# Optimization experiments

Measured on AMD Instinct MI355X. Metric: run time of the kernel, lower is better.

The kernel has to match this reference:

```python
import jax, jax.numpy as jnp
import numpy as np

B, S, H = 4, 2048, 1024

def setup_inputs() -> dict:
    key = jax.random.key(0)
    ks = jax.random.split(key, 6)
    scale = 1.0 / np.sqrt(H)
    return {
        "query": jax.random.normal(ks[0], (B, S, H), dtype=jnp.float32),
        "key":   jax.random.normal(ks[1], (B, S, H), dtype=jnp.float32),
        "value": jax.random.normal(ks[2], (B, S, H), dtype=jnp.float32),
        "Wq": jax.random.normal(ks[3], (H, H), dtype=jnp.float32) * scale,
        "Wk": jax.random.normal(ks[4], (H, H), dtype=jnp.float32) * scale,
        "Wv": jax.random.normal(ks[5], (H, H), dtype=jnp.float32) * scale,
    }

def reference(query, key, value, Wq, Wk, Wv):
    # nn.Linear(bias=False): y = x @ W.T
    q = jnp.einsum('bsh,oh->bso', query, Wq)
    k = jnp.einsum('bsh,oh->bso', key, Wk)
    v = jnp.einsum('bsh,oh->bso', value, Wv)
    # full QK^T scores [B, Q, K], scaled by sqrt(hidden_size)
    scores = jnp.einsum('bqh,bkh->bqk', q, k) / jnp.sqrt(jnp.asarray(H, q.dtype))
    attn = jax.nn.softmax(scores, axis=2)
    return jnp.einsum('bqk,bkh->bqh', attn, v)
```

## Files before the change

kernel.cpp:

```cpp
#include <hip/hip_runtime.h>
#include <hip/hip_bf16.h>
#include <stdint.h>

#define BATCH 4
#define SLEN  2048
#define HID   1024

typedef __attribute__((ext_vector_type(8))) short bfrag8;
typedef __attribute__((ext_vector_type(4))) float facc4;
typedef __attribute__((ext_vector_type(4))) unsigned short us4;

__device__ __forceinline__ unsigned short f2b(float f) {
  union { float f; unsigned int i; } x; x.f = f;
  unsigned int r = x.i + 0x7FFFu + ((x.i >> 16) & 1u);
  return (unsigned short)(r >> 16);
}

__device__ __forceinline__ void gl_lds16(const void* g, void* l) {
  __builtin_amdgcn_global_load_lds(
      (const __attribute__((address_space(1))) void*)g,
      (__attribute__((address_space(3))) void*)l, 16, 0, 0);
}

__global__ __launch_bounds__(256) void cast_all(
    const float* __restrict__ q, const float* __restrict__ k,
    const float* __restrict__ v, const float* __restrict__ wq,
    const float* __restrict__ wk, const float* __restrict__ wv,
    us4* __restrict__ dst, float* __restrict__ lsum) {
  if (blockIdx.x < 8) {
    float4 z = {0.f, 0.f, 0.f, 0.f};
    ((float4*)lsum)[blockIdx.x * 256 + threadIdx.x] = z;
  }
  const long i = (long)blockIdx.x * 256 + threadIdx.x;
  const long S1 = 2097152, S2 = 4194304, S3 = 6291456,
             S4 = 6553600, S5 = 6815744;
  const float4* src; long off;
  if (i < S2) {
    if (i < S1) { src = (const float4*)q;  off = i; }
    else        { src = (const float4*)k;  off = i - S1; }
  } else if (i < S3) { src = (const float4*)v;  off = i - S2; }
  else if   (i < S4) { src = (const float4*)wq; off = i - S3; }
  else if   (i < S5) { src = (const float4*)wk; off = i - S4; }
  else               { src = (const float4*)wv; off = i - S5; }
  float4 x = src[off];
  us4 o;
  o.x = f2b(x.x); o.y = f2b(x.y); o.z = f2b(x.z); o.w = f2b(x.w);
  dst[i] = o;
}

__global__ __launch_bounds__(256) void proj3(
    const unsigned short* __restrict__ Xq, const unsigned short* __restrict__ Wqb,
    const unsigned short* __restrict__ Xk, const unsigned short* __restrict__ Wkb,
    const unsigned short* __restrict__ Xv, const unsigned short* __restrict__ Wvb,
    unsigned short* __restrict__ Qb, unsigned short* __restrict__ Kb,
    unsigned short* __restrict__ Vt) {
  const int pid = blockIdx.x;
  const int p2     = (pid & 7) * 192 + (pid >> 3);
  const int g      = p2 >> 9;
  const int within = p2 & 511;

  const unsigned short* A; const unsigned short* B; unsigned short* C;
  long bm, bn; int ldc_;
  if (g == 0)      { A = Xq; B = Wqb; C = Qb; }
  else if (g == 1) { A = Xk; B = Wkb; C = Kb; }
  else             { A = Wvb; B = Xv; C = Vt; }
  if (g < 2) {
    const int gid = within >> 5, rem = within & 31;
    bm = (long)(gid * 4 + (rem & 3)) * 128;
    bn = (long)(rem >> 2) * 128;
    ldc_ = 1024;
  } else {
    const int gid = within >> 8, rem = within & 255;
    bm = (long)(gid * 4 + (rem & 3)) * 128;
    bn = (long)(rem >> 2) * 128;
    ldc_ = 8192;
  }

  __shared__ __align__(16) unsigned short As[128 * 64];
  __shared__ __align__(16) unsigned short Bs[128 * 64];

  const int tid  = threadIdx.x;
  const int lane = tid & 63;
  const int wave = tid >> 6;
  const int wr   = (wave >> 1) * 64;
  const int wc   = (wave & 1) * 64;
  const int ln   = lane & 15;
  const int lq   = lane >> 4;
  const int swz  = ln & 7;

  facc4 acc[4][4] = {};

  const unsigned short* ap[4]; const unsigned short* bp[4];
  unsigned short* asd[4]; unsigned short* bsd[4];
#pragma unroll
  for (int j = 0; j < 4; ++j) {
    const int c   = j * 256 + tid;
    const int row = c >> 3;
    const int src = ((c & 7) ^ (row & 7)) * 8;
    ap[j]  = A + (bm + row) * 1024 + src;
    bp[j]  = B + (bn + row) * 1024 + src;
    asd[j] = &As[c * 8];
    bsd[j] = &Bs[c * 8];
  }

  for (int k0 = 0; k0 < 1024; k0 += 64) {
#pragma unroll
    for (int j = 0; j < 4; ++j) { gl_lds16(ap[j], asd[j]); ap[j] += 64; }
#pragma unroll
    for (int j = 0; j < 4; ++j) { gl_lds16(bp[j], bsd[j]); bp[j] += 64; }
    __syncthreads();

#pragma unroll
    for (int kk = 0; kk < 2; ++kk) {
      bfrag8 af[4], bfr[4];
#pragma unroll
      for (int i = 0; i < 4; ++i)
        af[i] = *(const bfrag8*)&As[(wr + i * 16 + ln) * 64 + ((kk * 4 + lq) ^ swz) * 8];
#pragma unroll
      for (int j = 0; j < 4; ++j)
        bfr[j] = *(const bfrag8*)&Bs[(wc + j * 16 + ln) * 64 + ((kk * 4 + lq) ^ swz) * 8];
#pragma unroll
      for (int i = 0; i < 4; ++i)
#pragma unroll
        for (int j = 0; j < 4; ++j)
          acc[i][j] = __builtin_amdgcn_mfma_f32_16x16x32_bf16(af[i], bfr[j], acc[i][j], 0, 0, 0);
    }
    __syncthreads();
  }

#pragma unroll
  for (int i = 0; i < 4; ++i)
#pragma unroll
    for (int j = 0; j < 4; ++j) {
      const long m = bm + wr + i * 16 + lq * 4;
      const long n = bn + wc + j * 16 + ln;
#pragma unroll
      for (int r = 0; r < 4; ++r)
        C[(m + r) * (long)ldc_ + n] = f2b(acc[i][j][r]);
    }
}

template <int NT>
__device__ __forceinline__ void core256(
    const unsigned short* __restrict__ A, const unsigned short* __restrict__ B,
    const int lda, const int ldb,
    unsigned short* __restrict__ As, unsigned short* __restrict__ Bs,
    facc4 (&acc)[8][4]) {
  const int tid  = threadIdx.x;
  const int lane = tid & 63;
  const int wave = tid >> 6;
  const int wm = wave >> 2;
  const int wn = wave & 3;
  const int ln = lane & 15;
  const int lq = lane >> 4;
  const int swz = ln & 7;

  const int row0 = tid >> 3;
  const int blk  = (tid & 7) ^ (row0 & 7);
  const unsigned short* pA = A + (long)row0 * lda + blk * 8;
  const unsigned short* pB = B + (long)row0 * ldb + blk * 8;
  const long a64 = 64l * lda, b64 = 64l * ldb;
  unsigned short* dA = As + tid * 8;
  unsigned short* dB = Bs + tid * 8;

#define STG_A(h, b, t) do { const unsigned short* g_ = pA + (h) * (a64 * 2) + (long)(t) * 64; \
    gl_lds16(g_,       dA + (b) * 16384 + (h) * 8192); \
    gl_lds16(g_ + a64, dA + (b) * 16384 + (h) * 8192 + 4096); } while (0)
#define STG_B(h, b, t) do { const unsigned short* g_ = pB + (h) * (b64 * 2) + (long)(t) * 64; \
    gl_lds16(g_,       dB + (b) * 16384 + (h) * 8192); \
    gl_lds16(g_ + b64, dB + (b) * 16384 + (h) * 8192 + 4096); } while (0)

  const int o0 = (lq ^ swz) * 8;
  const int o1 = ((4 + lq) ^ swz) * 8;
  const int aOfs = wm * 8192 + ln * 64;
  const int bOfs = (wn >> 1) * 8192 + ((wn & 1) * 64 + ln) * 64;

#define RD_A4(dst, bufb, mb) do { \
  _Pragma("unroll") for (int m_ = 0; m_ < 4; ++m_) { \
    dst[m_][0] = *(const bfrag8*)(As + (bufb) + aOfs + ((mb) + m_) * 1024 + o0); \
    dst[m_][1] = *(const bfrag8*)(As + (bufb) + aOfs + ((mb) + m_) * 1024 + o1); \
  } } while (0)
#define RD_B2(dst, bufb, nb) do { \
  _Pragma("unroll") for (int n_ = 0; n_ < 2; ++n_) { \
    dst[n_][0] = *(const bfrag8*)(Bs + (bufb) + bOfs + ((nb) + n_) * 1024 + o0); \
    dst[n_][1] = *(const bfrag8*)(Bs + (bufb) + bOfs + ((nb) + n_) * 1024 + o1); \
  } } while (0)

#define MFMAQ(AF, BF, MO, NO) do { \
  _Pragma("unroll") for (int m_ = 0; m_ < 4; ++m_) \
  _Pragma("unroll") for (int n_ = 0; n_ < 2; ++n_) { \
    acc[(MO)+m_][(NO)+n_] = __builtin_amdgcn_mfma_f32_16x16x32_bf16( \
        AF[m_][0], BF[n_][0], acc[(MO)+m_][(NO)+n_], 0, 0, 0); \
    acc[(MO)+m_][(NO)+n_] = __builtin_amdgcn_mfma_f32_16x16x32_bf16( \
        AF[m_][1], BF[n_][1], acc[(MO)+m_][(NO)+n_], 0, 0, 0); \
  } } while (0)

#define PH_MID \
  __builtin_amdgcn_s_barrier(); \
  asm volatile("s_waitcnt lgkmcnt(0)" ::: "memory"); \
  __builtin_amdgcn_sched_barrier(0); \
  __builtin_amdgcn_s_setprio(1)
#define PH_END \
  __builtin_amdgcn_s_setprio(0); \
  __builtin_amdgcn_sched_barrier(0); \
  __builtin_amdgcn_s_barrier()

  STG_A(0, 0, 0); STG_A(1, 0, 0); STG_B(0, 0, 0); STG_B(1, 0, 0);
  STG_B(0, 1, 1); STG_B(1, 1, 1);
  asm volatile("s_waitcnt vmcnt(4)" ::: "memory");
  __builtin_amdgcn_s_barrier();

  constexpr int NI = NT / 2;
#pragma unroll 1
  for (int i = 0; i < NI - 1; ++i) {
    const int O1 = 2 * i + 1, E2 = 2 * i + 2, O2 = 2 * i + 3;
    {
      bfrag8 a0[4][2], a1[4][2], b0[2][2], b1[2][2];
      RD_A4(a0, 0, 0); RD_B2(b0, 0, 0); STG_A(0, 1, O1);
      PH_MID; MFMAQ(a0, b0, 0, 0); PH_END;
      RD_B2(b1, 0, 2); STG_A(1, 1, O1);
      PH_MID; MFMAQ(a0, b1, 0, 2); PH_END;
      RD_A4(a1, 0, 4); STG_B(0, 0, E2);
      PH_MID; MFMAQ(a1, b1, 4, 2); PH_END;
      STG_B(1, 0, E2);
      PH_MID; MFMAQ(a1, b0, 4, 0);
      __builtin_amdgcn_s_setprio(0);
      __builtin_amdgcn_sched_barrier(0);
      asm volatile("s_waitcnt vmcnt(4)" ::: "memory");
      __builtin_amdgcn_s_barrier();
    }
    {
      bfrag8 a0[4][2], a1[4][2], b0[2][2], b1[2][2];
      RD_A4(a0, 16384, 0); RD_B2(b0, 16384, 0); STG_A(0, 0, E2);
      PH_MID; MFMAQ(a0, b0, 0, 0); PH_END;
      RD_B2(b1, 16384, 2); STG_A(1, 0, E2);
      PH_MID; MFMAQ(a0, b1, 0, 2); PH_END;
      RD_A4(a1, 16384, 4); STG_B(0, 1, O2);
      PH_MID; MFMAQ(a1, b1, 4, 2); PH_END;
      STG_B(1, 1, O2);
      PH_MID; MFMAQ(a1, b0, 4, 0);
      __builtin_amdgcn_s_setprio(0);
      __builtin_amdgcn_sched_barrier(0);
      asm volatile("s_waitcnt vmcnt(4)" ::: "memory");
      __builtin_amdgcn_s_barrier();
    }
  }
  {
    const int O1 = NT - 1;
    {
      bfrag8 a0[4][2], a1[4][2], b0[2][2], b1[2][2];
      RD_A4(a0, 0, 0); RD_B2(b0, 0, 0); STG_A(0, 1, O1);
      PH_MID; MFMAQ(a0, b0, 0, 0); PH_END;
      RD_B2(b1, 0, 2); STG_A(1, 1, O1);
      PH_MID; MFMAQ(a0, b1, 0, 2); PH_END;
      RD_A4(a1, 0, 4);
      PH_MID; MFMAQ(a1, b1, 4, 2); PH_END;
      PH_MID; MFMAQ(a1, b0, 4, 0);
      __builtin_amdgcn_s_setprio(0);
      __builtin_amdgcn_sched_barrier(0);
      asm volatile("s_waitcnt vmcnt(0)" ::: "memory");
      __builtin_amdgcn_s_barrier();
    }
    {
      bfrag8 a0[4][2], a1[4][2], b0[2][2], b1[2][2];
      RD_A4(a0, 16384, 0); RD_B2(b0, 16384, 0);
      PH_MID; MFMAQ(a0, b0, 0, 0); PH_END;
      RD_B2(b1, 16384, 2);
      PH_MID; MFMAQ(a0, b1, 0, 2); PH_END;
      RD_A4(a1, 16384, 4);
      PH_MID; MFMAQ(a1, b1, 4, 2); PH_END;
      PH_MID; MFMAQ(a1, b0, 4, 0);
      __builtin_amdgcn_s_setprio(0);
    }
  }
#undef PH_MID
#undef PH_END
#undef MFMAQ
#undef RD_A4
#undef RD_B2
#undef STG_A
#undef STG_B
}

__global__ __launch_bounds__(512, 2) void scores256(
    const unsigned short* __restrict__ Q, const unsigned short* __restrict__ Kb,
    unsigned short* __restrict__ P, float* __restrict__ lsum) {
  extern __shared__ unsigned short smem[];
  unsigned short* As = smem;
  unsigned short* Bs = smem + 32768;

  const long z = blockIdx.z;
  const int pid = blockIdx.y * 8 + blockIdx.x;
  const int p2  = (pid & 7) * 8 + (pid >> 3);
  const long bm = (long)(p2 >> 3) * 256;
  const long bn = (long)(p2 & 7) * 256;

  const long SH = (long)SLEN * HID, SS = (long)SLEN * SLEN;
  facc4 acc[8][4] = {};
  core256<HID / 64>(Q + z * SH + bm * 1024, Kb + z * SH + bn * 1024, 1024, 1024,
                    As, Bs, acc);

  unsigned short* Pz = P + z * SS;
  float* lz = lsum + z * SLEN;
  const int lane = threadIdx.x & 63, wave = threadIdx.x >> 6;
  const int wm = wave >> 2, wn = wave & 3;
  const int ln = lane & 15, lq = lane >> 4;
#pragma unroll
  for (int m = 0; m < 8; ++m) {
#pragma unroll
    for (int r = 0; r < 4; ++r) {
      const long q = bm + wm * 128 + m * 16 + lq * 4 + r;
      float rowsum = 0.f;
#pragma unroll
      for (int n = 0; n < 4; ++n) {
        const long kcol = bn + wn * 64 + n * 16 + ln;
        float e = __expf(acc[m][n][r] * 0.03125f);
        Pz[q * (long)SLEN + kcol] = f2b(e);
        rowsum += e;
      }
      rowsum += __shfl_xor(rowsum, 1, 64);
      rowsum += __shfl_xor(rowsum, 2, 64);
      rowsum += __shfl_xor(rowsum, 4, 64);
      rowsum += __shfl_xor(rowsum, 8, 64);
      if (ln == 0) atomicAdd(&lz[q], rowsum);
    }
  }
}

template <int MODE, typename OutT>
__global__ __launch_bounds__(256) void gemm_nt(
    const unsigned short* __restrict__ A, const unsigned short* __restrict__ B,
    OutT* __restrict__ C, int K, int lda, int ldb, int ldc,
    long aStrideZ, long bStrideZ, long cStrideZ, float alpha,
    float* __restrict__ lsum) {
  A += (long)blockIdx.z * aStrideZ;
  B += (long)blockIdx.z * bStrideZ;
  C += (long)blockIdx.z * cStrideZ;
  const long lz = (long)blockIdx.z * SLEN;

  const int nbm = gridDim.x, nbn = gridDim.y;
  const int nb  = nbm * nbn;
  const int pid = blockIdx.y * nbm + blockIdx.x;
  const int p2  = (pid & 7) * (nb >> 3) + (pid >> 3);
  const int GROUP = 4;
  const int gsize = GROUP * nbn;
  const int gid   = p2 / gsize;
  const int rem   = p2 - gid * gsize;
  const long bm = (long)(gid * GROUP + (rem & (GROUP - 1))) * 128;
  const long bn = (long)(rem >> 2) * 128;

  __shared__ __align__(16) unsigned short As[128 * 64];
  __shared__ __align__(16) unsigned short Bs[128 * 64];

  const int tid  = threadIdx.x;
  const int lane = tid & 63;
  const int wave = tid >> 6;
  const int wr   = (wave >> 1) * 64;
  const int wc   = (wave & 1) * 64;
  const int ln   = lane & 15;
  const int lq   = lane >> 4;
  const int swz  = ln & 7;

  facc4 acc[4][4] = {};

  const unsigned short* ap[4]; const unsigned short* bp[4];
  unsigned short* asd[4]; unsigned short* bsd[4];
#pragma unroll
  for (int j = 0; j < 4; ++j) {
    const int c   = j * 256 + tid;
    const int row = c >> 3;
    const int src = ((c & 7) ^ (row & 7)) * 8;
    ap[j]  = A + (bm + row) * (long)lda + src;
    bp[j]  = B + (bn + row) * (long)ldb + src;
    asd[j] = &As[c * 8];
    bsd[j] = &Bs[c * 8];
  }

  for (int k0 = 0; k0 < K; k0 += 64) {
#pragma unroll
    for (int j = 0; j < 4; ++j) { gl_lds16(ap[j], asd[j]); ap[j] += 64; }
#pragma unroll
    for (int j = 0; j < 4; ++j) { gl_lds16(bp[j], bsd[j]); bp[j] += 64; }
    __syncthreads();

#pragma unroll
    for (int kk = 0; kk < 2; ++kk) {
      bfrag8 af[4], bfr[4];
#pragma unroll
      for (int i = 0; i < 4; ++i)
        af[i] = *(const bfrag8*)&As[(wr + i * 16 + ln) * 64 + ((kk * 4 + lq) ^ swz) * 8];
#pragma unroll
      for (int j = 0; j < 4; ++j)
        bfr[j] = *(const bfrag8*)&Bs[(wc + j * 16 + ln) * 64 + ((kk * 4 + lq) ^ swz) * 8];
#pragma unroll
      for (int i = 0; i < 4; ++i)
#pragma unroll
        for (int j = 0; j < 4; ++j)
          acc[i][j] = __builtin_amdgcn_mfma_f32_16x16x32_bf16(af[i], bfr[j], acc[i][j], 0, 0, 0);
    }
    __syncthreads();
  }

  if constexpr (MODE == 1) {
#pragma unroll
    for (int i = 0; i < 4; ++i) {
#pragma unroll
      for (int r = 0; r < 4; ++r) {
        const long m = bm + wr + i * 16 + lq * 4 + r;
        float rowsum = 0.f;
#pragma unroll
        for (int j = 0; j < 4; ++j) {
          const long n = bn + wc + j * 16 + ln;
          float e = __expf(acc[i][j][r] * alpha);
          C[m * (long)ldc + n] = (OutT)f2b(e);
          rowsum += e;
        }
        rowsum += __shfl_xor(rowsum, 1, 64);
        rowsum += __shfl_xor(rowsum, 2, 64);
        rowsum += __shfl_xor(rowsum, 4, 64);
        rowsum += __shfl_xor(rowsum, 8, 64);
        if (ln == 0) atomicAdd(&lsum[lz + m], rowsum);
      }
    }
  } else {
    float inv[16];
#pragma unroll
    for (int i = 0; i < 4; ++i)
#pragma unroll
      for (int r = 0; r < 4; ++r)
        inv[i * 4 + r] = 1.0f / lsum[lz + bm + wr + i * 16 + lq * 4 + r];
#pragma unroll
    for (int i = 0; i < 4; ++i)
#pragma unroll
      for (int j = 0; j < 4; ++j) {
        const long m = bm + wr + i * 16 + lq * 4;
        const long n = bn + wc + j * 16 + ln;
#pragma unroll
        for (int r = 0; r < 4; ++r)
          ((float*)C)[(m + r) * (long)ldc + n] = acc[i][j][r] * inv[i * 4 + r];
      }
  }
}

extern "C" void kernel_launch(void* const* d_in, const int* in_sizes, int n_in,
                              void* d_out, int out_size, void* d_ws, size_t ws_size,
                              hipStream_t stream) {
  const float* q_in = (const float*)d_in[0];
  const float* k_in = (const float*)d_in[1];
  const float* v_in = (const float*)d_in[2];
  const float* wq   = (const float*)d_in[3];
  const float* wk   = (const float*)d_in[4];
  const float* wv   = (const float*)d_in[5];
  float* out = (float*)d_out;

  const long NXH = (long)BATCH * SLEN * HID;
  const long NW  = (long)HID * HID;
  const long SH  = (long)SLEN * HID;
  const long SS  = (long)SLEN * SLEN;

  unsigned short* ws = (unsigned short*)d_ws;
  unsigned short* Xq  = ws;
  unsigned short* Xk  = Xq  + NXH;
  unsigned short* Xv  = Xk  + NXH;
  unsigned short* Wqb = Xv  + NXH;
  unsigned short* Wkb = Wqb + NW;
  unsigned short* Wvb = Wkb + NW;
  unsigned short* Qb  = Wvb + NW;
  unsigned short* Kb  = Qb  + NXH;
  unsigned short* Vt  = Kb  + NXH;
  float*          lsum = (float*)(Vt + NXH);
  unsigned short* P   = Xq;

  static bool attr_done = false;
  if (!attr_done) {
    hipFuncSetAttribute(reinterpret_cast<const void*>(scores256),
                        hipFuncAttributeMaxDynamicSharedMemorySize, 131072);
    attr_done = true;
  }

  cast_all<<<dim3(27648), dim3(256), 0, stream>>>(q_in, k_in, v_in, wq, wk, wv,
                                                  (us4*)ws, lsum);

  proj3<<<dim3(1536), dim3(256), 0, stream>>>(Xq, Wqb, Xk, Wkb, Xv, Wvb,
                                              Qb, Kb, Vt);

  scores256<<<dim3(8, 8, BATCH), dim3(512), 131072, stream>>>(Qb, Kb, P, lsum);

  gemm_nt<2, float><<<dim3(16, 8, BATCH), dim3(256), 0, stream>>>(
      P, Vt, out, SLEN, SLEN, BATCH * SLEN, HID, SS, SLEN, SH, 1.0f, lsum);
}
```

Measured before the change: 277.7 us.

## Fuse all four stages into one persistent cooperative kernel with grid syncs

Replaces the four separate launches (cast, projection, scores, PV) with one cooperative persistent kernel of 256 blocks × 512 threads that runs each stage in turn, separated by grid.sync(). Each block splits into two 256-thread halves to run the 128-tile projection and PV jobs. The aim is to remove launch gaps and inter-kernel drain and fill. In exchange, occupancy is fixed at 256 blocks, 131 KB of LDS is used even for the small-tile stages, and grid-wide barriers are added; a fallback path keeps the old multi-kernel launch if the cooperative launch fails.

```diff
diff --git a/kernel.cpp b/kernel.cpp
--- a/kernel.cpp
+++ b/kernel.cpp
@@ -1,6 +1,9 @@
 #include <hip/hip_runtime.h>
+#include <hip/hip_cooperative_groups.h>
 #include <hip/hip_bf16.h>
 #include <stdint.h>
+
+namespace cg = cooperative_groups;
 
 #define BATCH 4
 #define SLEN  2048
@@ -22,16 +25,12 @@
       (__attribute__((address_space(3))) void*)l, 16, 0, 0);
 }
 
-__global__ __launch_bounds__(256) void cast_all(
-    const float* __restrict__ q, const float* __restrict__ k,
+
+__device__ __forceinline__ void cast_elem(
+    long i, const float* __restrict__ q, const float* __restrict__ k,
     const float* __restrict__ v, const float* __restrict__ wq,
     const float* __restrict__ wk, const float* __restrict__ wv,
-    us4* __restrict__ dst, float* __restrict__ lsum) {
-  if (blockIdx.x < 8) {
-    float4 z = {0.f, 0.f, 0.f, 0.f};
-    ((float4*)lsum)[blockIdx.x * 256 + threadIdx.x] = z;
-  }
-  const long i = (long)blockIdx.x * 256 + threadIdx.x;
+    us4* __restrict__ dst) {
   const long S1 = 2097152, S2 = 4194304, S3 = 6291456,
              S4 = 6553600, S5 = 6815744;
   const float4* src; long off;
@@ -48,14 +47,14 @@
   dst[i] = o;
 }
 
-__global__ __launch_bounds__(256) void proj3(
+__device__ __forceinline__ void proj_job(
+    int p2, int tid,
+    unsigned short* __restrict__ As, unsigned short* __restrict__ Bs,
     const unsigned short* __restrict__ Xq, const unsigned short* __restrict__ Wqb,
     const unsigned short* __restrict__ Xk, const unsigned short* __restrict__ Wkb,
     const unsigned short* __restrict__ Xv, const unsigned short* __restrict__ Wvb,
     unsigned short* __restrict__ Qb, unsigned short* __restrict__ Kb,
     unsigned short* __restrict__ Vt) {
-  const int pid = blockIdx.x;
-  const int p2     = (pid & 7) * 192 + (pid >> 3);
   const int g      = p2 >> 9;
   const int within = p2 & 511;
 
@@ -76,10 +75,6 @@
     ldc_ = 8192;
   }
 
-  __shared__ __align__(16) unsigned short As[128 * 64];
-  __shared__ __align__(16) unsigned short Bs[128 * 64];
-
-  const int tid  = threadIdx.x;
   const int lane = tid & 63;
   const int wave = tid >> 6;
   const int wr   = (wave >> 1) * 64;
@@ -137,6 +132,82 @@
 #pragma unroll
       for (int r = 0; r < 4; ++r)
         C[(m + r) * (long)ldc_ + n] = f2b(acc[i][j][r]);
+    }
+}
+
+__device__ __forceinline__ void pv_job(
+    int tid, unsigned short* __restrict__ As, unsigned short* __restrict__ Bs,
+    const unsigned short* __restrict__ P, const unsigned short* __restrict__ Vt,
+    float* __restrict__ out, const float* __restrict__ lsum,
+    long z, long bm, long bn) {
+  const unsigned short* A = P  + z * (long)SLEN * SLEN;
+  const unsigned short* B = Vt + z * SLEN;
+  float* C = out + z * (long)SLEN * HID;
+  const float* lz = lsum + z * SLEN;
+
+  const int lane = tid & 63;
+  const int wave = tid >> 6;
+  const int wr   = (wave >> 1) * 64;
+  const int wc   = (wave & 1) * 64;
+  const int ln   = lane & 15;
+  const int lq   = lane >> 4;
+  const int swz  = ln & 7;
+
+  facc4 acc[4][4] = {};
+
+  const unsigned short* ap[4]; const unsigned short* bp[4];
+  unsigned short* asd[4]; unsigned short* bsd[4];
+#pragma unroll
+  for (int j = 0; j < 4; ++j) {
+    const int c   = j * 256 + tid;
+    const int row = c >> 3;
+    const int src = ((c & 7) ^ (row & 7)) * 8;
+    ap[j]  = A + (bm + row) * 2048l + src;
+    bp[j]  = B + (bn + row) * 8192l + src;
+    asd[j] = &As[c * 8];
+    bsd[j] = &Bs[c * 8];
+  }
+
+  for (int k0 = 0; k0 < 2048; k0 += 64) {
+#pragma unroll
+    for (int j = 0; j < 4; ++j) { gl_lds16(ap[j], asd[j]); ap[j] += 64; }
+#pragma unroll
+    for (int j = 0; j < 4; ++j) { gl_lds16(bp[j], bsd[j]); bp[j] += 64; }
+    __syncthreads();
+
+#pragma unroll
+    for (int kk = 0; kk < 2; ++kk) {
+      bfrag8 af[4], bfr[4];
+#pragma unroll
+      for (int i = 0; i < 4; ++i)
+        af[i] = *(const bfrag8*)&As[(wr + i * 16 + ln) * 64 + ((kk * 4 + lq) ^ swz) * 8];
+#pragma unroll
+      for (int j = 0; j < 4; ++j)
+        bfr[j] = *(const bfrag8*)&Bs[(wc + j * 16 + ln) * 64 + ((kk * 4 + lq) ^ swz) * 8];
+#pragma unroll
+      for (int i = 0; i < 4; ++i)
+#pragma unroll
+        for (int j = 0; j < 4; ++j)
+          acc[i][j] = __builtin_amdgcn_mfma_f32_16x16x32_bf16(af[i], bfr[j], acc[i][j], 0, 0, 0);
+    }
+    __syncthreads();
+  }
+
+  float inv[16];
+#pragma unroll
+  for (int i = 0; i < 4; ++i)
+#pragma unroll
+    for (int r = 0; r < 4; ++r)
+      inv[i * 4 + r] = 1.0f / lz[bm + wr + i * 16 + lq * 4 + r];
+#pragma unroll
+  for (int i = 0; i < 4; ++i)
+#pragma unroll
+    for (int j = 0; j < 4; ++j) {
+      const long m = bm + wr + i * 16 + lq * 4;
+      const long n = bn + wc + j * 16 + ln;
+#pragma unroll
+      for (int r = 0; r < 4; ++r)
+        C[(m + r) * 1024l + n] = acc[i][j][r] * inv[i * 4 + r];
     }
 }
 
@@ -282,22 +353,16 @@
 #undef STG_B
 }
 
-__global__ __launch_bounds__(512, 2) void scores256(
-    const unsigned short* __restrict__ Q, const unsigned short* __restrict__ Kb,
-    unsigned short* __restrict__ P, float* __restrict__ lsum) {
-  extern __shared__ unsigned short smem[];
+__device__ __forceinline__ void scores_job(
+    unsigned short* __restrict__ smem,
+    const unsigned short* __restrict__ Qb, const unsigned short* __restrict__ Kb,
+    unsigned short* __restrict__ P, float* __restrict__ lsum,
+    long z, long bm, long bn) {
   unsigned short* As = smem;
   unsigned short* Bs = smem + 32768;
-
-  const long z = blockIdx.z;
-  const int pid = blockIdx.y * 8 + blockIdx.x;
-  const int p2  = (pid & 7) * 8 + (pid >> 3);
-  const long bm = (long)(p2 >> 3) * 256;
-  const long bn = (long)(p2 & 7) * 256;
-
   const long SH = (long)SLEN * HID, SS = (long)SLEN * SLEN;
   facc4 acc[8][4] = {};
-  core256<HID / 64>(Q + z * SH + bm * 1024, Kb + z * SH + bn * 1024, 1024, 1024,
+  core256<HID / 64>(Qb + z * SH + bm * 1024, Kb + z * SH + bn * 1024, 1024, 1024,
                     As, Bs, acc);
 
   unsigned short* Pz = P + z * SS;
@@ -309,156 +374,33 @@
   for (int m = 0; m < 8; ++m) {
 #pragma unroll
     for (int r = 0; r < 4; ++r) {
-      const long q = bm + wm * 128 + m * 16 + lq * 4 + r;
+      const long qrow = bm + wm * 128 + m * 16 + lq * 4 + r;
       float rowsum = 0.f;
 #pragma unroll
       for (int n = 0; n < 4; ++n) {
         const long kcol = bn + wn * 64 + n * 16 + ln;
         float e = __expf(acc[m][n][r] * 0.03125f);
-        Pz[q * (long)SLEN + kcol] = f2b(e);
+        Pz[qrow * (long)SLEN + kcol] = f2b(e);
         rowsum += e;
       }
       rowsum += __shfl_xor(rowsum, 1, 64);
       rowsum += __shfl_xor(rowsum, 2, 64);
       rowsum += __shfl_xor(rowsum, 4, 64);
       rowsum += __shfl_xor(rowsum, 8, 64);
-      if (ln == 0) atomicAdd(&lz[q], rowsum);
-    }
-  }
-}
-
-template <int MODE, typename OutT>
-__global__ __launch_bounds__(256) void gemm_nt(
-    const unsigned short* __restrict__ A, const unsigned short* __restrict__ B,
-    OutT* __restrict__ C, int K, int lda, int ldb, int ldc,
-    long aStrideZ, long bStrideZ, long cStrideZ, float alpha,
-    float* __restrict__ lsum) {
-  A += (long)blockIdx.z * aStrideZ;
-  B += (long)blockIdx.z * bStrideZ;
-  C += (long)blockIdx.z * cStrideZ;
-  const long lz = (long)blockIdx.z * SLEN;
-
-  const int nbm = gridDim.x, nbn = gridDim.y;
-  const int nb  = nbm * nbn;
-  const int pid = blockIdx.y * nbm + blockIdx.x;
-  const int p2  = (pid & 7) * (nb >> 3) + (pid >> 3);
-  const int GROUP = 4;
-  const int gsize = GROUP * nbn;
-  const int gid   = p2 / gsize;
-  const int rem   = p2 - gid * gsize;
-  const long bm = (long)(gid * GROUP + (rem & (GROUP - 1))) * 128;
-  const long bn = (long)(rem >> 2) * 128;
-
-  __shared__ __align__(16) unsigned short As[128 * 64];
-  __shared__ __align__(16) unsigned short Bs[128 * 64];
-
-  const int tid  = threadIdx.x;
-  const int lane = tid & 63;
-  const int wave = tid >> 6;
-  const int wr   = (wave >> 1) * 64;
-  const int wc   = (wave & 1) * 64;
-  const int ln   = lane & 15;
-  const int lq   = lane >> 4;
-  const int swz  = ln & 7;
-
-  facc4 acc[4][4] = {};
-
-  const unsigned short* ap[4]; const unsigned short* bp[4];
-  unsigned short* asd[4]; unsigned short* bsd[4];
-#pragma unroll
-  for (int j = 0; j < 4; ++j) {
-    const int c   = j * 256 + tid;
-    const int row = c >> 3;
-    const int src = ((c & 7) ^ (row & 7)) * 8;
-    ap[j]  = A + (bm + row) * (long)lda + src;
-    bp[j]  = B + (bn + row) * (long)ldb + src;
-    asd[j] = &As[c * 8];
-    bsd[j] = &Bs[c * 8];
-  }
-
-  for (int k0 = 0; k0 < K; k0 += 64) {
-#pragma unroll
-    for (int j = 0; j < 4; ++j) { gl_lds16(ap[j], asd[j]); ap[j] += 64; }
-#pragma unroll
-    for (int j = 0; j < 4; ++j) { gl_lds16(bp[j], bsd[j]); bp[j] += 64; }
-    __syncthreads();
-
-#pragma unroll
-    for (int kk = 0; kk < 2; ++kk) {
-      bfrag8 af[4], bfr[4];
-#pragma unroll
-      for (int i = 0; i < 4; ++i)
-        af[i] = *(const bfrag8*)&As[(wr + i * 16 + ln) * 64 + ((kk * 4 + lq) ^ swz) * 8];
-#pragma unroll
-      for (int j = 0; j < 4; ++j)
-        bfr[j] = *(const bfrag8*)&Bs[(wc + j * 16 + ln) * 64 + ((kk * 4 + lq) ^ swz) * 8];
-#pragma unroll
-      for (int i = 0; i < 4; ++i)
-#pragma unroll
-        for (int j = 0; j < 4; ++j)
-          acc[i][j] = __builtin_amdgcn_mfma_f32_16x16x32_bf16(af[i], bfr[j], acc[i][j], 0, 0, 0);
-    }
-    __syncthreads();
-  }
-
-  if constexpr (MODE == 1) {
-#pragma unroll
-    for (int i = 0; i < 4; ++i) {
-#pragma unroll
-      for (int r = 0; r < 4; ++r) {
-        const long m = bm + wr + i * 16 + lq * 4 + r;
-        float rowsum = 0.f;
-#pragma unroll
-        for (int j = 0; j < 4; ++j) {
-          const long n = bn + wc + j * 16 + ln;
-          float e = __expf(acc[i][j][r] * alpha);
-          C[m * (long)ldc + n] = (OutT)f2b(e);
-          rowsum += e;
-        }
-        rowsum += __shfl_xor(rowsum, 1, 64);
-        rowsum += __shfl_xor(rowsum, 2, 64);
-        rowsum += __shfl_xor(rowsum, 4, 64);
-        rowsum += __shfl_xor(rowsum, 8, 64);
-        if (ln == 0) atomicAdd(&lsum[lz + m], rowsum);
-      }
-    }
-  } else {
-    float inv[16];
-#pragma unroll
-    for (int i = 0; i < 4; ++i)
-#pragma unroll
-      for (int r = 0; r < 4; ++r)
-        inv[i * 4 + r] = 1.0f / lsum[lz + bm + wr + i * 16 + lq * 4 + r];
-#pragma unroll
-    for (int i = 0; i < 4; ++i)
-#pragma unroll
-      for (int j = 0; j < 4; ++j) {
-        const long m = bm + wr + i * 16 + lq * 4;
-        const long n = bn + wc + j * 16 + ln;
-#pragma unroll
-        for (int r = 0; r < 4; ++r)
-          ((float*)C)[(m + r) * (long)ldc + n] = acc[i][j][r] * inv[i * 4 + r];
-      }
-  }
-}
-
-extern "C" void kernel_launch(void* const* d_in, const int* in_sizes, int n_in,
-                              void* d_out, int out_size, void* d_ws, size_t ws_size,
-                              hipStream_t stream) {
-  const float* q_in = (const float*)d_in[0];
-  const float* k_in = (const float*)d_in[1];
-  const float* v_in = (const float*)d_in[2];
-  const float* wq   = (const float*)d_in[3];
-  const float* wk   = (const float*)d_in[4];
-  const float* wv   = (const float*)d_in[5];
-  float* out = (float*)d_out;
+      if (ln == 0) atomicAdd(&lz[qrow], rowsum);
+    }
+  }
+}
+
+__global__ __launch_bounds__(512, 2) void fused_all(
+    const float* __restrict__ q_in, const float* __restrict__ k_in,
+    const float* __restrict__ v_in, const float* __restrict__ wq,
+    const float* __restrict__ wk, const float* __restrict__ wv,
+    float* __restrict__ out, unsigned short* __restrict__ ws) {
+  extern __shared__ unsigned short smem[];
 
   const long NXH = (long)BATCH * SLEN * HID;
   const long NW  = (long)HID * HID;
-  const long SH  = (long)SLEN * HID;
-  const long SS  = (long)SLEN * SLEN;
-
-  unsigned short* ws = (unsigned short*)d_ws;
   unsigned short* Xq  = ws;
   unsigned short* Xk  = Xq  + NXH;
   unsigned short* Xv  = Xk  + NXH;
@@ -471,21 +413,157 @@
   float*          lsum = (float*)(Vt + NXH);
   unsigned short* P   = Xq;
 
+  cg::grid_group grid = cg::this_grid();
+
+  {
+    const long gid = (long)blockIdx.x * 512 + threadIdx.x;
+    if (gid < 2048) {
+      float4 z4 = {0.f, 0.f, 0.f, 0.f};
+      ((float4*)lsum)[gid] = z4;
+    }
+    us4* dst = (us4*)ws;
+    const long TOT = 7077888;
+#pragma unroll 1
+    for (long i = gid; i < TOT; i += 131072)
+      cast_elem(i, q_in, k_in, v_in, wq, wk, wv, dst);
+  }
+  grid.sync();
+
+  {
+    const int half = threadIdx.x >> 8;
+    const int tid  = threadIdx.x & 255;
+    unsigned short* As = smem + half * 16384;
+    unsigned short* Bs = As + 8192;
+    const int base = (blockIdx.x & 7) * 192 + (blockIdx.x >> 3) * 6 + half * 3;
+#pragma unroll 1
+    for (int j = 0; j < 3; ++j)
+      proj_job(base + j, tid, As, Bs, Xq, Wqb, Xk, Wkb, Xv, Wvb, Qb, Kb, Vt);
+  }
+  grid.sync();
+
+  {
+    const long z  = blockIdx.x >> 6;
+    const int pid = blockIdx.x & 63;
+    const int p2  = (pid & 7) * 8 + (pid >> 3);
+    const long bm = (long)(p2 >> 3) * 256;
+    const long bn = (long)(p2 & 7) * 256;
+    scores_job(smem, Qb, Kb, P, lsum, z, bm, bn);
+  }
+  grid.sync();
+
+  {
+    const int half = threadIdx.x >> 8;
+    const int tid  = threadIdx.x & 255;
+    unsigned short* As = smem + half * 16384;
+    unsigned short* Bs = As + 8192;
+    const int unit   = (blockIdx.x >> 3) * 2 + half;
+    const int jobidx = (blockIdx.x & 7) * 64 + unit;
+    const long z = jobidx >> 7;
+    const int within = jobidx & 63;
+    const long bm = (long)(((jobidx >> 6) & 1) * 8 +
+                           (within >> 5) * 4 + (within & 3)) * 128;
+    const long bn = (long)((within >> 2) & 7) * 128;
+    pv_job(tid, As, Bs, P, Vt, out, lsum, z, bm, bn);
+  }
+}
+
+__global__ __launch_bounds__(256) void cast_all(
+    const float* __restrict__ q, const float* __restrict__ k,
+    const float* __restrict__ v, const float* __restrict__ wq,
+    const float* __restrict__ wk, const float* __restrict__ wv,
+    us4* __restrict__ dst, float* __restrict__ lsum) {
+  if (blockIdx.x < 8) {
+    float4 z = {0.f, 0.f, 0.f, 0.f};
+    ((float4*)lsum)[blockIdx.x * 256 + threadIdx.x] = z;
+  }
+  const long i = (long)blockIdx.x * 256 + threadIdx.x;
+  cast_elem(i, q, k, v, wq, wk, wv, dst);
+}
+
+__global__ __launch_bounds__(256) void proj3(
+    const unsigned short* __restrict__ Xq, const unsigned short* __restrict__ Wqb,
+    const unsigned short* __restrict__ Xk, const unsigned short* __restrict__ Wkb,
+    const unsigned short* __restrict__ Xv, const unsigned short* __restrict__ Wvb,
+    unsigned short* __restrict__ Qb, unsigned short* __restrict__ Kb,
+    unsigned short* __restrict__ Vt) {
+  __shared__ __align__(16) unsigned short As[128 * 64];
+  __shared__ __align__(16) unsigned short Bs[128 * 64];
+  const int p2 = (blockIdx.x & 7) * 192 + (blockIdx.x >> 3);
+  proj_job(p2, threadIdx.x, As, Bs, Xq, Wqb, Xk, Wkb, Xv, Wvb, Qb, Kb, Vt);
+}
+
+__global__ __launch_bounds__(512, 2) void scores256(
+    const unsigned short* __restrict__ Q, const unsigned short* __restrict__ Kb,
+    unsigned short* __restrict__ P, float* __restrict__ lsum) {
+  extern __shared__ unsigned short smem[];
+  const long z = blockIdx.z;
+  const int pid = blockIdx.y * 8 + blockIdx.x;
+  const int p2  = (pid & 7) * 8 + (pid >> 3);
+  scores_job(smem, Q, Kb, P, lsum, z, (long)(p2 >> 3) * 256, (long)(p2 & 7) * 256);
+}
+
+__global__ __launch_bounds__(256) void pv128(
+    const unsigned short* __restrict__ P, const unsigned short* __restrict__ Vt,
+    float* __restrict__ out, const float* __restrict__ lsum) {
+  __shared__ __align__(16) unsigned short As[128 * 64];
+  __shared__ __align__(16) unsigned short Bs[128 * 64];
+  const int pid = blockIdx.y * 16 + blockIdx.x;
+  const int p2  = (pid & 7) * 16 + (pid >> 3);
+  const int gid = p2 >> 5, rem = p2 & 31;
+  const long bm = (long)(gid * 4 + (rem & 3)) * 128;
+  const long bn = (long)(rem >> 2) * 128;
+  pv_job(threadIdx.x, As, Bs, P, Vt, out, lsum, (long)blockIdx.z, bm, bn);
+}
+
+extern "C" void kernel_launch(void* const* d_in, const int* in_sizes, int n_in,
+                              void* d_out, int out_size, void* d_ws, size_t ws_size,
+                              hipStream_t stream) {
+  const float* q_in = (const float*)d_in[0];
+  const float* k_in = (const float*)d_in[1];
+  const float* v_in = (const float*)d_in[2];
+  const float* wq   = (const float*)d_in[3];
+  const float* wk   = (const float*)d_in[4];
+  const float* wv   = (const float*)d_in[5];
+  float* out = (float*)d_out;
+  unsigned short* ws = (unsigned short*)d_ws;
+
+  const long NXH = (long)BATCH * SLEN * HID;
+  const long NW  = (long)HID * HID;
+
   static bool attr_done = false;
   if (!attr_done) {
+    hipFuncSetAttribute(reinterpret_cast<const void*>(fused_all),
+                        hipFuncAttributeMaxDynamicSharedMemorySize, 131072);
     hipFuncSetAttribute(reinterpret_cast<const void*>(scores256),
                         hipFuncAttributeMaxDynamicSharedMemorySize, 131072);
     attr_done = true;
   }
 
-  cast_all<<<dim3(27648), dim3(256), 0, stream>>>(q_in, k_in, v_in, wq, wk, wv,
-                                                  (us4*)ws, lsum);
-
-  proj3<<<dim3(1536), dim3(256), 0, stream>>>(Xq, Wqb, Xk, Wkb, Xv, Wvb,
-                                              Qb, Kb, Vt);
-
-  scores256<<<dim3(8, 8, BATCH), dim3(512), 131072, stream>>>(Qb, Kb, P, lsum);
-
-  gemm_nt<2, float><<<dim3(16, 8, BATCH), dim3(256), 0, stream>>>(
-      P, Vt, out, SLEN, SLEN, BATCH * SLEN, HID, SS, SLEN, SH, 1.0f, lsum);
-}
+  void* params[] = {(void*)&q_in, (void*)&k_in, (void*)&v_in,
+                    (void*)&wq,   (void*)&wk,   (void*)&wv,
+                    (void*)&out,  (void*)&ws};
+  hipError_t ce = hipLaunchCooperativeKernel(
+      reinterpret_cast<const void*>(fused_all), dim3(256), dim3(512),
+      params, 131072, stream);
+  if (ce != hipSuccess) {
+    (void)hipGetLastError();
+    unsigned short* Xq  = ws;
+    unsigned short* Xk  = Xq  + NXH;
+    unsigned short* Xv  = Xk  + NXH;
+    unsigned short* Wqb = Xv  + NXH;
+    unsigned short* Wkb = Wqb + NW;
+    unsigned short* Wvb = Wkb + NW;
+    unsigned short* Qb  = Wvb + NW;
+    unsigned short* Kb  = Qb  + NXH;
+    unsigned short* Vt  = Kb  + NXH;
+    float*          lsum = (float*)(Vt + NXH);
+    unsigned short* P   = Xq;
+
+    cast_all<<<dim3(27648), dim3(256), 0, stream>>>(q_in, k_in, v_in, wq, wk, wv,
+                                                    (us4*)ws, lsum);
+    proj3<<<dim3(1536), dim3(256), 0, stream>>>(Xq, Wqb, Xk, Wkb, Xv, Wvb,
+                                                Qb, Kb, Vt);
+    scores256<<<dim3(8, 8, BATCH), dim3(512), 131072, stream>>>(Qb, Kb, P, lsum);
+    pv128<<<dim3(16, 8, BATCH), dim3(256), 0, stream>>>(P, Vt, out, lsum);
+  }
+}
```

Result: slower. 453.4 us (+63.3%).

## Replace generic PV GEMM with 256x128-tile double-buffered pipelined kernel

Applied to the files above, without the earlier changes.

Replaces the generic 128x128 single-buffered gemm_nt used for the P·V product with a dedicated pv256 kernel. It uses 512 threads, 256x128 output tiles and double-buffered LDS holding 64-wide K slabs. Global-to-LDS loads of the next slab are interleaved with MFMA quarter-phases, using explicit vmcnt waits, barriers and priority hints. The aim is to hide memory latency behind compute and raise operand reuse per tile. In exchange the grid shrinks to 256 blocks, which could leave some compute units underused, and the hand-scheduled barriers make correctness fragile.

```diff
diff --git a/kernel.cpp b/kernel.cpp
--- a/kernel.cpp
+++ b/kernel.cpp
@@ -327,118 +327,172 @@
   }
 }
 
-template <int MODE, typename OutT>
-__global__ __launch_bounds__(256) void gemm_nt(
-    const unsigned short* __restrict__ A, const unsigned short* __restrict__ B,
-    OutT* __restrict__ C, int K, int lda, int ldb, int ldc,
-    long aStrideZ, long bStrideZ, long cStrideZ, float alpha,
-    float* __restrict__ lsum) {
-  A += (long)blockIdx.z * aStrideZ;
-  B += (long)blockIdx.z * bStrideZ;
-  C += (long)blockIdx.z * cStrideZ;
-  const long lz = (long)blockIdx.z * SLEN;
-
-  const int nbm = gridDim.x, nbn = gridDim.y;
-  const int nb  = nbm * nbn;
-  const int pid = blockIdx.y * nbm + blockIdx.x;
-  const int p2  = (pid & 7) * (nb >> 3) + (pid >> 3);
-  const int GROUP = 4;
-  const int gsize = GROUP * nbn;
-  const int gid   = p2 / gsize;
-  const int rem   = p2 - gid * gsize;
-  const long bm = (long)(gid * GROUP + (rem & (GROUP - 1))) * 128;
-  const long bn = (long)(rem >> 2) * 128;
-
-  __shared__ __align__(16) unsigned short As[128 * 64];
-  __shared__ __align__(16) unsigned short Bs[128 * 64];
+__global__ __launch_bounds__(512, 2) void pv256(
+    const unsigned short* __restrict__ P, const unsigned short* __restrict__ Vt,
+    float* __restrict__ out, const float* __restrict__ lsum) {
+  extern __shared__ unsigned short smem[];
+  unsigned short* As = smem;
+  unsigned short* Bs = smem + 32768;
+
+  const long z  = blockIdx.z;
+  const int pid = blockIdx.y * 8 + blockIdx.x;
+  const int p2  = (pid & 7) * 8 + (pid >> 3);
+  const long bm = (long)(p2 >> 3) * 256;
+  const long bn = (long)(p2 & 7) * 128;
+
+  const unsigned short* A = P  + z * (long)SLEN * SLEN + bm * 2048;
+  const unsigned short* B = Vt + z * SLEN + bn * 8192;
+  float* C = out + z * (long)SLEN * HID;
+  const float* lz = lsum + z * SLEN;
 
   const int tid  = threadIdx.x;
   const int lane = tid & 63;
   const int wave = tid >> 6;
-  const int wr   = (wave >> 1) * 64;
-  const int wc   = (wave & 1) * 64;
-  const int ln   = lane & 15;
-  const int lq   = lane >> 4;
-  const int swz  = ln & 7;
+  const int wm = wave >> 1;
+  const int wn = wave & 1;
+  const int ln = lane & 15;
+  const int lq = lane >> 4;
+  const int swz = ln & 7;
+
+  const int row0 = tid >> 3;
+  const int blk  = (tid & 7) ^ (row0 & 7);
+  const unsigned short* pA = A + (long)row0 * 2048 + blk * 8;
+  const unsigned short* pB = B + (long)row0 * 8192 + blk * 8;
+  const long a64 = 64l * 2048, b64 = 64l * 8192;
+  unsigned short* dA = As + tid * 8;
+  unsigned short* dB = Bs + tid * 8;
+
+#define PSTG_A(h, b, t) do { const unsigned short* g_ = pA + (h) * (a64 * 2) + (long)(t) * 64; \
+    gl_lds16(g_,       dA + (b) * 16384 + (h) * 8192); \
+    gl_lds16(g_ + a64, dA + (b) * 16384 + (h) * 8192 + 4096); } while (0)
+#define PSTG_B(b, t) do { const unsigned short* g_ = pB + (long)(t) * 64; \
+    gl_lds16(g_,       dB + (b) * 8192); \
+    gl_lds16(g_ + b64, dB + (b) * 8192 + 4096); } while (0)
+
+  const int o0 = (lq ^ swz) * 8;
+  const int o1 = ((4 + lq) ^ swz) * 8;
+  const int aOfs = wm * 4096 + ln * 64;
+  const int bOfs = wn * 4096 + ln * 64;
+
+#define PRD_A(dst, bufb, mb) do { \
+  _Pragma("unroll") for (int m_ = 0; m_ < 2; ++m_) { \
+    dst[m_][0] = *(const bfrag8*)(As + (bufb) + aOfs + ((mb) + m_) * 1024 + o0); \
+    dst[m_][1] = *(const bfrag8*)(As + (bufb) + aOfs + ((mb) + m_) * 1024 + o1); \
+  } } while (0)
+#define PRD_B(dst, bufb, nb) do { \
+  _Pragma("unroll") for (int n_ = 0; n_ < 2; ++n_) { \
+    dst[n_][0] = *(const bfrag8*)(Bs + (bufb) + bOfs + ((nb) + n_) * 1024 + o0); \
+    dst[n_][1] = *(const bfrag8*)(Bs + (bufb) + bOfs + ((nb) + n_) * 1024 + o1); \
+  } } while (0)
 
   facc4 acc[4][4] = {};
-
-  const unsigned short* ap[4]; const unsigned short* bp[4];
-  unsigned short* asd[4]; unsigned short* bsd[4];
-#pragma unroll
-  for (int j = 0; j < 4; ++j) {
-    const int c   = j * 256 + tid;
-    const int row = c >> 3;
-    const int src = ((c & 7) ^ (row & 7)) * 8;
-    ap[j]  = A + (bm + row) * (long)lda + src;
-    bp[j]  = B + (bn + row) * (long)ldb + src;
-    asd[j] = &As[c * 8];
-    bsd[j] = &Bs[c * 8];
-  }
-
-  for (int k0 = 0; k0 < K; k0 += 64) {
-#pragma unroll
-    for (int j = 0; j < 4; ++j) { gl_lds16(ap[j], asd[j]); ap[j] += 64; }
-#pragma unroll
-    for (int j = 0; j < 4; ++j) { gl_lds16(bp[j], bsd[j]); bp[j] += 64; }
-    __syncthreads();
-
-#pragma unroll
-    for (int kk = 0; kk < 2; ++kk) {
-      bfrag8 af[4], bfr[4];
-#pragma unroll
-      for (int i = 0; i < 4; ++i)
-        af[i] = *(const bfrag8*)&As[(wr + i * 16 + ln) * 64 + ((kk * 4 + lq) ^ swz) * 8];
-#pragma unroll
-      for (int j = 0; j < 4; ++j)
-        bfr[j] = *(const bfrag8*)&Bs[(wc + j * 16 + ln) * 64 + ((kk * 4 + lq) ^ swz) * 8];
-#pragma unroll
-      for (int i = 0; i < 4; ++i)
-#pragma unroll
-        for (int j = 0; j < 4; ++j)
-          acc[i][j] = __builtin_amdgcn_mfma_f32_16x16x32_bf16(af[i], bfr[j], acc[i][j], 0, 0, 0);
-    }
-    __syncthreads();
-  }
-
-  if constexpr (MODE == 1) {
-#pragma unroll
-    for (int i = 0; i < 4; ++i) {
-#pragma unroll
-      for (int r = 0; r < 4; ++r) {
-        const long m = bm + wr + i * 16 + lq * 4 + r;
-        float rowsum = 0.f;
-#pragma unroll
-        for (int j = 0; j < 4; ++j) {
-          const long n = bn + wc + j * 16 + ln;
-          float e = __expf(acc[i][j][r] * alpha);
-          C[m * (long)ldc + n] = (OutT)f2b(e);
-          rowsum += e;
-        }
-        rowsum += __shfl_xor(rowsum, 1, 64);
-        rowsum += __shfl_xor(rowsum, 2, 64);
-        rowsum += __shfl_xor(rowsum, 4, 64);
-        rowsum += __shfl_xor(rowsum, 8, 64);
-        if (ln == 0) atomicAdd(&lsum[lz + m], rowsum);
-      }
-    }
-  } else {
-    float inv[16];
-#pragma unroll
-    for (int i = 0; i < 4; ++i)
+#define PMFMAQ(AF, BF, MO, NO) do { \
+  _Pragma("unroll") for (int m_ = 0; m_ < 2; ++m_) \
+  _Pragma("unroll") for (int n_ = 0; n_ < 2; ++n_) { \
+    acc[(MO)+m_][(NO)+n_] = __builtin_amdgcn_mfma_f32_16x16x32_bf16( \
+        AF[m_][0], BF[n_][0], acc[(MO)+m_][(NO)+n_], 0, 0, 0); \
+    acc[(MO)+m_][(NO)+n_] = __builtin_amdgcn_mfma_f32_16x16x32_bf16( \
+        AF[m_][1], BF[n_][1], acc[(MO)+m_][(NO)+n_], 0, 0, 0); \
+  } } while (0)
+
+#define PH_MID \
+  __builtin_amdgcn_s_barrier(); \
+  asm volatile("s_waitcnt lgkmcnt(0)" ::: "memory"); \
+  __builtin_amdgcn_sched_barrier(0); \
+  __builtin_amdgcn_s_setprio(1)
+#define PH_END \
+  __builtin_amdgcn_s_setprio(0); \
+  __builtin_amdgcn_sched_barrier(0); \
+  __builtin_amdgcn_s_barrier()
+
+  PSTG_A(0, 0, 0); PSTG_A(1, 0, 0); PSTG_B(0, 0);
+  PSTG_B(1, 1);
+  asm volatile("s_waitcnt vmcnt(2)" ::: "memory");
+  __builtin_amdgcn_s_barrier();
+
+  constexpr int NT = 32;
+#pragma unroll 1
+  for (int i = 0; i < NT / 2 - 1; ++i) {
+    const int O1 = 2 * i + 1, E2 = 2 * i + 2, O2 = 2 * i + 3;
+    {
+      bfrag8 a0[2][2], a1[2][2], b0[2][2], b1[2][2];
+      PRD_A(a0, 0, 0); PRD_B(b0, 0, 0); PSTG_A(0, 1, O1);
+      PH_MID; PMFMAQ(a0, b0, 0, 0); PH_END;
+      PRD_B(b1, 0, 2); PSTG_A(1, 1, O1);
+      PH_MID; PMFMAQ(a0, b1, 0, 2); PH_END;
+      PRD_A(a1, 0, 2); PSTG_B(0, E2);
+      PH_MID; PMFMAQ(a1, b1, 2, 2); PH_END;
+      PH_MID; PMFMAQ(a1, b0, 2, 0);
+      __builtin_amdgcn_s_setprio(0);
+      __builtin_amdgcn_sched_barrier(0);
+      asm volatile("s_waitcnt vmcnt(2)" ::: "memory");
+      __builtin_amdgcn_s_barrier();
+    }
+    {
+      bfrag8 a0[2][2], a1[2][2], b0[2][2], b1[2][2];
+      PRD_A(a0, 16384, 0); PRD_B(b0, 8192, 0); PSTG_A(0, 0, E2);
+      PH_MID; PMFMAQ(a0, b0, 0, 0); PH_END;
+      PRD_B(b1, 8192, 2); PSTG_A(1, 0, E2);
+      PH_MID; PMFMAQ(a0, b1, 0, 2); PH_END;
+      PRD_A(a1, 16384, 2); PSTG_B(1, O2);
+      PH_MID; PMFMAQ(a1, b1, 2, 2); PH_END;
+      PH_MID; PMFMAQ(a1, b0, 2, 0);
+      __builtin_amdgcn_s_setprio(0);
+      __builtin_amdgcn_sched_barrier(0);
+      asm volatile("s_waitcnt vmcnt(2)" ::: "memory");
+      __builtin_amdgcn_s_barrier();
+    }
+  }
+  {
+    const int O1 = NT - 1;
+    {
+      bfrag8 a0[2][2], a1[2][2], b0[2][2], b1[2][2];
+      PRD_A(a0, 0, 0); PRD_B(b0, 0, 0); PSTG_A(0, 1, O1);
+      PH_MID; PMFMAQ(a0, b0, 0, 0); PH_END;
+      PRD_B(b1, 0, 2); PSTG_A(1, 1, O1);
+      PH_MID; PMFMAQ(a0, b1, 0, 2); PH_END;
+      PRD_A(a1, 0, 2);
+      PH_MID; PMFMAQ(a1, b1, 2, 2); PH_END;
+      PH_MID; PMFMAQ(a1, b0, 2, 0);
+      __builtin_amdgcn_s_setprio(0);
+      __builtin_amdgcn_sched_barrier(0);
+      asm volatile("s_waitcnt vmcnt(0)" ::: "memory");
+      __builtin_amdgcn_s_barrier();
+    }
+    {
+      bfrag8 a0[2][2], a1[2][2], b0[2][2], b1[2][2];
+      PRD_A(a0, 16384, 0); PRD_B(b0, 8192, 0);
+      PH_MID; PMFMAQ(a0, b0, 0, 0); PH_END;
+      PRD_B(b1, 8192, 2);
+      PH_MID; PMFMAQ(a0, b1, 0, 2); PH_END;
+      PRD_A(a1, 16384, 2);
+      PH_MID; PMFMAQ(a1, b1, 2, 2); PH_END;
+      PH_MID; PMFMAQ(a1, b0, 2, 0);
+      __builtin_amdgcn_s_setprio(0);
+    }
+  }
+#undef PH_MID
+#undef PH_END
+#undef PMFMAQ
+#undef PRD_A
+#undef PRD_B
+#undef PSTG_A
+#undef PSTG_B
+
+#pragma unroll
+  for (int m = 0; m < 4; ++m) {
+    float inv[4];
+#pragma unroll
+    for (int r = 0; r < 4; ++r)
+      inv[r] = 1.0f / lz[bm + wm * 64 + m * 16 + lq * 4 + r];
+#pragma unroll
+    for (int n = 0; n < 4; ++n) {
+      const long mm = bm + wm * 64 + m * 16 + lq * 4;
+      const long nn = bn + wn * 64 + n * 16 + ln;
 #pragma unroll
       for (int r = 0; r < 4; ++r)
-        inv[i * 4 + r] = 1.0f / lsum[lz + bm + wr + i * 16 + lq * 4 + r];
-#pragma unroll
-    for (int i = 0; i < 4; ++i)
-#pragma unroll
-      for (int j = 0; j < 4; ++j) {
-        const long m = bm + wr + i * 16 + lq * 4;
-        const long n = bn + wc + j * 16 + ln;
-#pragma unroll
-        for (int r = 0; r < 4; ++r)
-          ((float*)C)[(m + r) * (long)ldc + n] = acc[i][j][r] * inv[i * 4 + r];
-      }
+        C[(mm + r) * 1024l + nn] = acc[m][n][r] * inv[r];
+    }
   }
 }
 
@@ -455,8 +509,6 @@
 
   const long NXH = (long)BATCH * SLEN * HID;
   const long NW  = (long)HID * HID;
-  const long SH  = (long)SLEN * HID;
-  const long SS  = (long)SLEN * SLEN;
 
   unsigned short* ws = (unsigned short*)d_ws;
   unsigned short* Xq  = ws;
@@ -475,6 +527,8 @@
   if (!attr_done) {
     hipFuncSetAttribute(reinterpret_cast<const void*>(scores256),
                         hipFuncAttributeMaxDynamicSharedMemorySize, 131072);
+    hipFuncSetAttribute(reinterpret_cast<const void*>(pv256),
+                        hipFuncAttributeMaxDynamicSharedMemorySize, 98304);
     attr_done = true;
   }
 
@@ -486,6 +540,5 @@
 
   scores256<<<dim3(8, 8, BATCH), dim3(512), 131072, stream>>>(Qb, Kb, P, lsum);
 
-  gemm_nt<2, float><<<dim3(16, 8, BATCH), dim3(256), 0, stream>>>(
-      P, Vt, out, SLEN, SLEN, BATCH * SLEN, HID, SS, SLEN, SH, 1.0f, lsum);
-}
+  pv256<<<dim3(8, 8, BATCH), dim3(512), 98304, stream>>>(P, Vt, out, lsum);
+}
```

Result: no change. 280.6 us (+1.1%).
